# Kernel tuning notes

Measured on AMD Instinct MI355X. Metric: run time of the kernel, lower is better.

## Reference

```python
import jax, jax.numpy as jnp
import numpy as np

N_HEAD = 16
ROPE_BASE = 10000.0

def _rotate_half(x):
    # matches torch: stack((-x[...,1::2], x[...,::2]), -1).flatten(-2)
    x1 = x[..., ::2]
    x2 = x[..., 1::2]
    return jnp.stack((-x2, x1), axis=-1).reshape(x.shape)

def setup_inputs() -> dict:
    key = jax.random.key(0)
    ks = jax.random.split(key, 5)
    B, T, C = 4, 2048, 1024
    x = jax.random.normal(ks[0], (B, T, C), dtype=jnp.float32)
    Wq = jax.random.normal(ks[1], (C, C), dtype=jnp.float32) * 0.02
    Wk = jax.random.normal(ks[2], (C, C), dtype=jnp.float32) * 0.02
    Wv = jax.random.normal(ks[3], (C, C), dtype=jnp.float32) * 0.02
    Wp = jax.random.normal(ks[4], (C, C), dtype=jnp.float32) * 0.02
    return {"x": x, "Wq": Wq, "Wk": Wk, "Wv": Wv, "Wp": Wp, "start_pos": 0}

def reference(x, Wq, Wk, Wv, Wp, start_pos):
    B, T, C = x.shape
    H = N_HEAD
    D = C // H
    # torch Linear: out = x @ W^T
    q = jnp.einsum('btc,dc->btd', x, Wq).reshape(B, T, H, D).transpose(0, 2, 1, 3)
    k = jnp.einsum('btc,dc->btd', x, Wk).reshape(B, T, H, D).transpose(0, 2, 1, 3)
    v = jnp.einsum('btc,dc->btd', x, Wv).reshape(B, T, H, D).transpose(0, 2, 1, 3)
    # RoPE cache (cat[freqs, freqs] with interleaved rotate_half, as in source)
    inv_freq = 1.0 / (ROPE_BASE ** (jnp.arange(0, D, 2, dtype=jnp.float32) / D))
    t = jnp.arange(T, dtype=jnp.float32) + jnp.float32(start_pos)
    freqs = t[:, None] * inv_freq[None, :]          # [T, D/2]
    emb = jnp.concatenate([freqs, freqs], axis=-1)  # [T, D]
    cos = jnp.cos(emb)[None, None]                  # [1,1,T,D]
    sin = jnp.sin(emb)[None, None]
    q = q * cos + _rotate_half(q) * sin
    k = k * cos + _rotate_half(k) * sin
    att = jnp.einsum('bhqd,bhkd->bhqk', q, k) / jnp.sqrt(jnp.float32(D))
    mask = jnp.triu(jnp.ones((T, T), dtype=bool), k=1)
    att = jnp.where(mask, -jnp.inf, att)
    att = jax.nn.softmax(att, axis=-1)
    y = jnp.einsum('bhqk,bhkd->bhqd', att, v)
    y = y.transpose(0, 2, 1, 3).reshape(B, T, C)
    return jnp.einsum('btc,dc->btd', y, Wp)
```

## Files before the change

kernel.cpp:

```cpp
#include <hip/hip_runtime.h>
#include <hip/hip_bf16.h>
#include <stdint.h>

#define B_  4
#define T_  2048
#define C_  1024
#define H_  16
#define D_  64
#define BT  (B_*T_)
#define KDIM 1024

typedef __attribute__((ext_vector_type(8))) short bf16x8;
typedef __attribute__((ext_vector_type(4))) float f32x4;

__device__ __forceinline__ unsigned short f2bf(float f) {
  union { float f; unsigned u; } v; v.f = f;
  unsigned r = v.u + 0x7FFFu + ((v.u >> 16) & 1u);
  return (unsigned short)(r >> 16);
}

__device__ __forceinline__ float exp2_fast(float x) {
  float r;
  asm("v_exp_f32 %0, %1" : "=v"(r) : "v"(x));
  return r;
}

__device__ __forceinline__ void gld_lds16(const void* g, void* l) {
  __builtin_amdgcn_global_load_lds(
      (__attribute__((address_space(1))) unsigned int*)(uintptr_t)g,
      (__attribute__((address_space(3))) unsigned int*)(unsigned)(uintptr_t)l,
      16, 0, 0);
}

__global__ __launch_bounds__(256) void k_convert(
    const float* __restrict__ x,  const float* __restrict__ wq,
    const float* __restrict__ wk, const float* __restrict__ wv,
    const float* __restrict__ wp,
    unsigned short* __restrict__ xb, unsigned short* __restrict__ wcat,
    unsigned short* __restrict__ wpb)
{
  const int NX = BT*C_/4;
  const int NW = C_*C_/4;
  const int TOT = NX + 4*NW;
  for (int i = blockIdx.x*blockDim.x + threadIdx.x; i < TOT; i += gridDim.x*blockDim.x) {
    const float4* src; unsigned short* dst; int idx;
    if (i < NX)                { src = (const float4*)x;  dst = xb;            idx = i; }
    else {
      int j = i - NX;
      if (j < NW)              { src = (const float4*)wq; dst = wcat;          idx = j; }
      else if (j < 2*NW)       { src = (const float4*)wk; dst = wcat + C_*C_;  idx = j - NW; }
      else if (j < 3*NW)       { src = (const float4*)wv; dst = wcat + 2*C_*C_;idx = j - 2*NW; }
      else                     { src = (const float4*)wp; dst = wpb;           idx = j - 3*NW; }
    }
    float4 v = src[idx];
    ushort4 o; o.x = f2bf(v.x); o.y = f2bf(v.y); o.z = f2bf(v.z); o.w = f2bf(v.w);
    *(ushort4*)(dst + (size_t)idx*4) = o;
  }
}

__global__ __launch_bounds__(256) void k_rope_tab(
    const int* __restrict__ start_pos, float* __restrict__ cosT, float* __restrict__ sinT)
{
  int i = blockIdx.x*blockDim.x + threadIdx.x;
  if (i >= T_*D_) return;
  int t = i >> 6, j = i & 63;
  float inv = exp2f(-(float)(j & 31) * (13.287712379549449f / 32.0f));
  float ang = (float)(t + start_pos[0]) * inv;
  cosT[i] = cosf(ang);
  sinT[i] = sinf(ang);
}

__global__ __launch_bounds__(1024, 4) void k_gemm256(
    const unsigned short* __restrict__ A, const unsigned short* __restrict__ Bw,
    unsigned short* __restrict__ qb, unsigned short* __restrict__ kb,
    unsigned short* __restrict__ vt,
    const float* __restrict__ cosT, const float* __restrict__ sinT)
{
  __shared__ __attribute__((aligned(16))) char smem[114688];
  const int tid = threadIdx.x, l = tid & 63, w = tid >> 6;
  const int g = l >> 4, c = l & 15;
  const int m0 = blockIdx.x * 256, n0 = blockIdx.y * 192;
  const int wr = w >> 2, wc = w & 3;
  const char* gA = (const char*)A;
  const char* gB = (const char*)Bw;

  int dstA[2]; size_t aoff[2];
#pragma unroll
  for (int j = 0; j < 2; ++j) {
    int P = j*16384 + tid*16;
    int row = P >> 7;
    int kc = ((P & 127) ^ ((row & 7) << 4)) >> 1;
    dstA[j] = P;
    aoff[j] = ((size_t)(m0 + row) * KDIM + kc) * 2;
  }
  int dstB[2]; size_t boff[2];
#pragma unroll
  for (int j = 0; j < 2; ++j) {
    int P = (j == 0) ? tid*16 : (16384 + tid*16);
    int row = P >> 7;
    int kc = ((P & 127) ^ ((row & 7) << 4)) >> 1;
    dstB[j] = P;
    boff[j] = ((size_t)(n0 + row) * KDIM + kc) * 2;
  }
  const bool bsec = (tid < 512);

  const int aB = (wr*64 + c) * 128;
  const int bB = 32768 + (wc*48 + c) * 128;
  const int xsw = (c & 7) << 4;

  f32x4 acc[4][3];
#pragma unroll
  for (int i = 0; i < 4; ++i)
#pragma unroll
    for (int j = 0; j < 3; ++j) acc[i][j] = (f32x4){0.f,0.f,0.f,0.f};

#pragma unroll
  for (int j = 0; j < 2; ++j) gld_lds16(gA + aoff[j], smem + dstA[j]);
  gld_lds16(gB + boff[0], smem + 32768 + dstB[0]);
  if (bsec) gld_lds16(gB + boff[1], smem + 32768 + dstB[1]);

  for (int t = 0; t < 16; ++t) {
    const int par = (t & 1) ? 57344 : 0;
    const int nxt = (t & 1) ? 0 : 57344;

    __syncthreads();

    if (t + 1 < 16) {
      const size_t ko = (size_t)(t + 1) * 128;
#pragma unroll
      for (int j = 0; j < 2; ++j) gld_lds16(gA + aoff[j] + ko, smem + nxt + dstA[j]);
      gld_lds16(gB + boff[0] + ko, smem + nxt + 32768 + dstB[0]);
      if (bsec) gld_lds16(gB + boff[1] + ko, smem + nxt + 32768 + dstB[1]);
    }

#pragma unroll
    for (int kk = 0; kk < 2; ++kk) {
      const int xt = (kk*64 + g*16) ^ xsw;
      bf16x8 af[4], bk[3];
#pragma unroll
      for (int ni = 0; ni < 3; ++ni)
        bk[ni] = *(const bf16x8*)(smem + par + bB + ni*2048 + xt);
#pragma unroll
      for (int mi = 0; mi < 4; ++mi)
        af[mi] = *(const bf16x8*)(smem + par + aB + mi*2048 + xt);
      __builtin_amdgcn_s_setprio(1);
#pragma unroll
      for (int mi = 0; mi < 4; ++mi)
#pragma unroll
        for (int ni = 0; ni < 3; ++ni)
          acc[mi][ni] = __builtin_amdgcn_mfma_f32_16x16x32_bf16(af[mi], bk[ni], acc[mi][ni], 0, 0, 0);
      __builtin_amdgcn_s_setprio(0);
    }
  }

#pragma unroll
  for (int mi = 0; mi < 4; ++mi) {
#pragma unroll
    for (int ni = 0; ni < 3; ++ni) {
      const int mrow0 = m0 + wr*64 + mi*16 + g*4;
      const int ncol  = n0 + wc*48 + ni*16 + c;
      const int which = ncol >> 10;
      const int d = ncol & 1023, h = d >> 6, dd = d & 63;
      const int b = mrow0 >> 11, t0 = mrow0 & 2047;
      if (which == 2) {
        ushort4 o;
        o.x = f2bf(acc[mi][ni][0]); o.y = f2bf(acc[mi][ni][1]);
        o.z = f2bf(acc[mi][ni][2]); o.w = f2bf(acc[mi][ni][3]);
        *(ushort4*)(vt + ((size_t)((b*H_ + h)*D_ + dd))*T_ + t0) = o;
      } else {
#pragma unroll
        for (int r = 0; r < 4; ++r) {
          float val = acc[mi][ni][r];
          float partner = __shfl_xor(val, 1);
          float rot = (dd & 1) ? partner : -partner;
          float cv = cosT[(t0 + r)*64 + dd], sv = sinT[(t0 + r)*64 + dd];
          float o = val*cv + rot*sv;
          size_t oidx = (((size_t)(b*H_ + h))*T_ + (t0 + r))*D_ + dd;
          if (which == 0) qb[oidx] = f2bf(o * 0.180336879f);
          else            kb[oidx] = f2bf(o);
        }
      }
    }
  }
}

__global__ __launch_bounds__(512, 4) void k_gemm1(
    const unsigned short* __restrict__ A, const unsigned short* __restrict__ Bw,
    float* __restrict__ outF)
{
  __shared__ __attribute__((aligned(16))) char smem[65536];
  const int tid = threadIdx.x, l = tid & 63, w = tid >> 6;
  const int g = l >> 4, c = l & 15;
  const int m0 = blockIdx.x * 128, n0 = blockIdx.y * 128;
  const int wr = w >> 2, wc = w & 3;
  const char* gA = (const char*)A;
  const char* gB = (const char*)Bw;

  int dstP[2]; size_t aoff[2], boff[2];
#pragma unroll
  for (int j = 0; j < 2; ++j) {
    int P = j*8192 + tid*16;
    int row = P >> 7;
    int kc = ((P & 127) ^ ((row & 7) << 4)) >> 1;
    dstP[j] = P;
    aoff[j] = ((size_t)(m0 + row) * KDIM + kc) * 2;
    boff[j] = ((size_t)(n0 + row) * KDIM + kc) * 2;
  }

  const int aB = (wr*64 + c) * 128;
  const int bB = 16384 + (wc*32 + c) * 128;
  const int xsw = (c & 7) << 4;

  f32x4 acc[4][2];
#pragma unroll
  for (int i = 0; i < 4; ++i)
#pragma unroll
    for (int j = 0; j < 2; ++j) acc[i][j] = (f32x4){0.f,0.f,0.f,0.f};

#pragma unroll
  for (int j = 0; j < 2; ++j) {
    gld_lds16(gA + aoff[j], smem + dstP[j]);
    gld_lds16(gB + boff[j], smem + 16384 + dstP[j]);
  }

  for (int t = 0; t < 16; ++t) {
    const int par = (t & 1) << 15;
    const int nxt = par ^ 32768;

    __syncthreads();

    if (t + 1 < 16) {
      const size_t ko = (size_t)(t + 1) * 128;
#pragma unroll
      for (int j = 0; j < 2; ++j) {
        gld_lds16(gA + aoff[j] + ko, smem + nxt + dstP[j]);
        gld_lds16(gB + boff[j] + ko, smem + nxt + 16384 + dstP[j]);
      }
    }

#pragma unroll
    for (int kk = 0; kk < 2; ++kk) {
      const int xt = (kk*64 + g*16) ^ xsw;
      bf16x8 af[4], bk[2];
#pragma unroll
      for (int ni = 0; ni < 2; ++ni)
        bk[ni] = *(const bf16x8*)(smem + par + bB + ni*2048 + xt);
#pragma unroll
      for (int mi = 0; mi < 4; ++mi)
        af[mi] = *(const bf16x8*)(smem + par + aB + mi*2048 + xt);
      __builtin_amdgcn_s_setprio(1);
#pragma unroll
      for (int mi = 0; mi < 4; ++mi)
#pragma unroll
        for (int ni = 0; ni < 2; ++ni)
          acc[mi][ni] = __builtin_amdgcn_mfma_f32_16x16x32_bf16(af[mi], bk[ni], acc[mi][ni], 0, 0, 0);
      __builtin_amdgcn_s_setprio(0);
    }
  }

#pragma unroll
  for (int mi = 0; mi < 4; ++mi) {
#pragma unroll
    for (int ni = 0; ni < 2; ++ni) {
      const int mrow0 = m0 + wr*64 + mi*16 + g*4;
      const int ncol  = n0 + wc*32 + ni*16 + c;
#pragma unroll
      for (int r = 0; r < 4; ++r)
        outF[(size_t)(mrow0 + r) * 1024 + ncol] = acc[mi][ni][r];
    }
  }
}

__global__ __launch_bounds__(512) void k_attn(
    const unsigned short* __restrict__ qb, const unsigned short* __restrict__ kb,
    const unsigned short* __restrict__ vt, unsigned short* __restrict__ yb)
{
  __shared__ __attribute__((aligned(16))) char smem[49152];
  const int tid = threadIdx.x, l = tid & 63, w = tid >> 6;
  const int g = l >> 4, c = l & 15;
  const int bh = blockIdx.x;
  const int pidx = blockIdx.y;
  const size_t bhO = (size_t)bh * T_ * D_;
  const int pbase = 32768 + w*2048;
  const int b = bh >> 4, h = bh & 15;

  bf16x8 vones;
#pragma unroll
  for (int i = 0; i < 8; ++i) vones[i] = (short)0x3F80;

  const char* srcK; const char* srcV; int dstP2;
  {
    int P = w*1024 + l*16;
    int row = P >> 7;
    int Lb = P ^ ((row & 7) << 4);
    int col = (Lb & 127) >> 1;
    dstP2 = P;
    srcK = (const char*)(kb + bhO) + ((size_t)row*D_ + col)*2;
    srcV = (const char*)(vt + bhO) + ((size_t)row*T_ + col)*2;
  }

  for (int half = 0; half < 2; ++half) {
    const int qt = half ? pidx : (15 - pidx);
    const int q0 = qt * 128;
    const int q0w = q0 + w*16;

    bf16x8 aq[2];
#pragma unroll
    for (int kc = 0; kc < 2; ++kc)
      aq[kc] = *(const bf16x8*)(qb + bhO + (size_t)(q0w + c)*D_ + kc*32 + g*8);

    f32x4 po[4];
    f32x4 ls;
    float mrun = -1e30f;
#pragma unroll
    for (int nd = 0; nd < 4; ++nd) po[nd] = (f32x4){0.f,0.f,0.f,0.f};
    ls = (f32x4){0.f,0.f,0.f,0.f};

    const int nkt = (q0 + 128) >> 6;

    gld_lds16(srcK, smem + dstP2);
    gld_lds16(srcV, smem + 8192 + dstP2);
    asm volatile("s_waitcnt vmcnt(0)" ::: "memory");
    __builtin_amdgcn_s_barrier();
    __builtin_amdgcn_sched_barrier(0);

    for (int it = 0; it < nkt; ++it) {
      const int kv0 = it * 64;
      const int cur = (it & 1) * 16384;
      const bool staging = (it + 1 < nkt);

      if (staging) {
        const int wb = 16384 - cur;
        gld_lds16(srcK + (size_t)(kv0 + 64) * 128, smem + wb + dstP2);
        gld_lds16(srcV + (size_t)(kv0 + 64) * 2,   smem + wb + 8192 + dstP2);
      }

      if (kv0 < q0w + 16) {
        f32x4 st[4];
#pragma unroll
        for (int ni = 0; ni < 4; ++ni) st[ni] = (f32x4){0.f,0.f,0.f,0.f};
        __builtin_amdgcn_s_setprio(1);
#pragma unroll
        for (int kk = 0; kk < 2; ++kk) {
          bf16x8 bk[4];
#pragma unroll
          for (int ni = 0; ni < 4; ++ni) {
            int kn = ni*16 + c;
            int Lb = kn*128 + (kk*32 + g*8)*2;
            bk[ni] = *(const bf16x8*)(smem + cur + (Lb ^ ((kn & 7) << 4)));
          }
#pragma unroll
          for (int ni = 0; ni < 4; ++ni)
            st[ni] = __builtin_amdgcn_mfma_f32_16x16x32_bf16(bk[ni], aq[kk], st[ni], 0, 0, 0);
        }
        __builtin_amdgcn_s_setprio(0);

        if (kv0 + 64 > q0w) {
          const int qq = q0w + c;
#pragma unroll
          for (int ni = 0; ni < 4; ++ni)
#pragma unroll
            for (int r = 0; r < 4; ++r) {
              int kvv = kv0 + ni*16 + g*4 + r;
              if (kvv > qq) st[ni][r] = -1e30f;
            }
        }

        {
          float mn[4];
#pragma unroll
          for (int ni = 0; ni < 4; ++ni)
            mn[ni] = fmaxf(fmaxf(st[ni][0], st[ni][1]), fmaxf(st[ni][2], st[ni][3]));
          float mt = fmaxf(fmaxf(mn[0], mn[1]), fmaxf(mn[2], mn[3]));
          mt = fmaxf(mt, __shfl_xor(mt, 16));
          mt = fmaxf(mt, __shfl_xor(mt, 32));
          float m_use = mrun;
          if (__any(mt > m_use + 8.f)) {
            float mnew = fmaxf(m_use, mt);
            float alpha = exp2_fast(m_use - mnew);
            mrun = mnew;
            m_use = mnew;
#pragma unroll
            for (int r = 0; r < 4; ++r) ls[r] *= alpha;
#pragma unroll
            for (int nd = 0; nd < 4; ++nd)
#pragma unroll
              for (int r = 0; r < 4; ++r) po[nd][r] *= alpha;
          }
#pragma unroll
          for (int ni = 0; ni < 4; ++ni)
#pragma unroll
            for (int r = 0; r < 4; ++r)
              st[ni][r] = exp2_fast(st[ni][r] - m_use);
        }

        {
          const int row = c;
          const int sw = (row & 7) << 4;
          const int rb = pbase + row*128;
#pragma unroll
          for (int ni = 0; ni < 4; ++ni) {
            unsigned u0, u1;
            asm("v_cvt_pk_bf16_f32 %0, %1, %2" : "=v"(u0) : "v"(st[ni][0]), "v"(st[ni][1]));
            asm("v_cvt_pk_bf16_f32 %0, %1, %2" : "=v"(u1) : "v"(st[ni][2]), "v"(st[ni][3]));
            int Lb = (ni*16 + g*4) * 2;
            uint2 uu; uu.x = u0; uu.y = u1;
            *(uint2*)(smem + rb + (Lb ^ sw)) = uu;
          }
        }

        __builtin_amdgcn_s_setprio(1);
#pragma unroll
        for (int kk = 0; kk < 2; ++kk) {
          bf16x8 pb;
          {
            int pr = c;
            int Lb = pr*128 + (kk*32 + g*8)*2;
            pb = *(const bf16x8*)(smem + pbase + (Lb ^ ((pr & 7) << 4)));
          }
          ls = __builtin_amdgcn_mfma_f32_16x16x32_bf16(vones, pb, ls, 0, 0, 0);
          bf16x8 bv[4];
#pragma unroll
          for (int nd = 0; nd < 4; ++nd) {
            int vr = nd*16 + c;
            int Lb = vr*128 + (kk*32 + g*8)*2;
            bv[nd] = *(const bf16x8*)(smem + cur + 8192 + (Lb ^ ((vr & 7) << 4)));
          }
#pragma unroll
          for (int nd = 0; nd < 4; ++nd)
            po[nd] = __builtin_amdgcn_mfma_f32_16x16x32_bf16(bv[nd], pb, po[nd], 0, 0, 0);
        }
        __builtin_amdgcn_s_setprio(0);
      }

      if (staging) { asm volatile("s_waitcnt vmcnt(0)" ::: "memory"); }
      __builtin_amdgcn_s_barrier();
      __builtin_amdgcn_sched_barrier(0);
    }

    {
      float inv = 1.f / ls[0];
      int t = q0w + c;
#pragma unroll
      for (int nd = 0; nd < 4; ++nd) {
        ushort4 o;
        o.x = f2bf(po[nd][0] * inv);
        o.y = f2bf(po[nd][1] * inv);
        o.z = f2bf(po[nd][2] * inv);
        o.w = f2bf(po[nd][3] * inv);
        *(ushort4*)(yb + ((size_t)b*T_ + t)*C_ + h*64 + nd*16 + g*4) = o;
      }
    }
  }
}

extern "C" void kernel_launch(void* const* d_in, const int* in_sizes, int n_in,
                              void* d_out, int out_size, void* d_ws, size_t ws_size,
                              hipStream_t stream)
{
  const float* x  = (const float*)d_in[0];
  const float* Wq = (const float*)d_in[1];
  const float* Wk = (const float*)d_in[2];
  const float* Wv = (const float*)d_in[3];
  const float* Wp = (const float*)d_in[4];
  const int*   sp = (const int*)d_in[5];
  float* out = (float*)d_out;

  char* ws = (char*)d_ws;
  unsigned short* xb   = (unsigned short*)(ws);
  unsigned short* wcat = (unsigned short*)(ws + 16777216);
  unsigned short* wpb  = (unsigned short*)(ws + 23068672);
  unsigned short* qb   = (unsigned short*)(ws + 25165824);
  unsigned short* kb   = (unsigned short*)(ws + 41943040);
  unsigned short* vt   = (unsigned short*)(ws + 58720256);
  unsigned short* yb   = (unsigned short*)(ws + 75497472);
  float* cosT = (float*)(ws + 92274688);
  float* sinT = (float*)(ws + 92798976);

  k_convert<<<dim3(2048), dim3(256), 0, stream>>>(x, Wq, Wk, Wv, Wp, xb, wcat, wpb);
  k_rope_tab<<<dim3(512), dim3(256), 0, stream>>>(sp, cosT, sinT);
  k_gemm256<<<dim3(32, 16), dim3(1024), 0, stream>>>(xb, wcat, qb, kb, vt, cosT, sinT);
  k_attn<<<dim3(64, 8), dim3(512), 0, stream>>>(qb, kb, vt, yb);
  k_gemm1<<<dim3(64, 8), dim3(512), 0, stream>>>(yb, wpb, out);
}
```

Measured before the change: 161.0 us.

## Give each attention wave 32 query rows and drop paired-tile balancing

Each attention block now handles one 256-row query tile instead of two balanced 128-row tiles. Each wave owns two 16-row subtiles, so every K and V fragment read from shared memory feeds twice as many MFMAs. Per-wave shared memory for the probability buffer doubles and the block's shared allocation grows to 64KB. The cost is more accumulator registers and the loss of the front/back pairing that evened out causal work across blocks; tiles are now issued heaviest first instead.

```diff
diff --git a/kernel.cpp b/kernel.cpp
--- a/kernel.cpp
+++ b/kernel.cpp
@@ -275,13 +275,13 @@
     const unsigned short* __restrict__ qb, const unsigned short* __restrict__ kb,
     const unsigned short* __restrict__ vt, unsigned short* __restrict__ yb)
 {
-  __shared__ __attribute__((aligned(16))) char smem[49152];
+  __shared__ __attribute__((aligned(16))) char smem[65536];
   const int tid = threadIdx.x, l = tid & 63, w = tid >> 6;
   const int g = l >> 4, c = l & 15;
   const int bh = blockIdx.x;
-  const int pidx = blockIdx.y;
+  const int qt = 7 - (int)blockIdx.y;
   const size_t bhO = (size_t)bh * T_ * D_;
-  const int pbase = 32768 + w*2048;
+  const int pbase = 32768 + w*4096;
   const int b = bh >> 4, h = bh & 15;
 
   bf16x8 vones;
@@ -299,157 +299,175 @@
     srcV = (const char*)(vt + bhO) + ((size_t)row*T_ + col)*2;
   }
 
-  for (int half = 0; half < 2; ++half) {
-    const int qt = half ? pidx : (15 - pidx);
-    const int q0 = qt * 128;
-    const int q0w = q0 + w*16;
-
-    bf16x8 aq[2];
+  const int q0 = qt * 256;
+  const int q0w = q0 + w*32;
+
+  bf16x8 aq[2][2];
+#pragma unroll
+  for (int mi = 0; mi < 2; ++mi)
 #pragma unroll
     for (int kc = 0; kc < 2; ++kc)
-      aq[kc] = *(const bf16x8*)(qb + bhO + (size_t)(q0w + c)*D_ + kc*32 + g*8);
-
-    f32x4 po[4];
-    f32x4 ls;
-    float mrun = -1e30f;
-#pragma unroll
-    for (int nd = 0; nd < 4; ++nd) po[nd] = (f32x4){0.f,0.f,0.f,0.f};
-    ls = (f32x4){0.f,0.f,0.f,0.f};
-
-    const int nkt = (q0 + 128) >> 6;
-
-    gld_lds16(srcK, smem + dstP2);
-    gld_lds16(srcV, smem + 8192 + dstP2);
-    asm volatile("s_waitcnt vmcnt(0)" ::: "memory");
+      aq[mi][kc] = *(const bf16x8*)(qb + bhO + (size_t)(q0w + mi*16 + c)*D_ + kc*32 + g*8);
+
+  f32x4 po[4][2];
+  f32x4 ls[2];
+  float mrun[2];
+#pragma unroll
+  for (int nd = 0; nd < 4; ++nd)
+#pragma unroll
+    for (int mi = 0; mi < 2; ++mi) po[nd][mi] = (f32x4){0.f,0.f,0.f,0.f};
+  ls[0] = (f32x4){0.f,0.f,0.f,0.f}; ls[1] = (f32x4){0.f,0.f,0.f,0.f};
+  mrun[0] = mrun[1] = -1e30f;
+
+  const int nkt = (q0 + 256) >> 6;
+
+  gld_lds16(srcK, smem + dstP2);
+  gld_lds16(srcV, smem + 8192 + dstP2);
+  asm volatile("s_waitcnt vmcnt(0)" ::: "memory");
+  __builtin_amdgcn_s_barrier();
+  __builtin_amdgcn_sched_barrier(0);
+
+  for (int it = 0; it < nkt; ++it) {
+    const int kv0 = it * 64;
+    const int cur = (it & 1) * 16384;
+    const bool staging = (it + 1 < nkt);
+
+    if (staging) {
+      const int wb = 16384 - cur;
+      gld_lds16(srcK + (size_t)(kv0 + 64) * 128, smem + wb + dstP2);
+      gld_lds16(srcV + (size_t)(kv0 + 64) * 2,   smem + wb + 8192 + dstP2);
+    }
+
+    if (kv0 < q0w + 32) {
+      f32x4 st[4][2];
+#pragma unroll
+      for (int ni = 0; ni < 4; ++ni)
+#pragma unroll
+        for (int mi = 0; mi < 2; ++mi) st[ni][mi] = (f32x4){0.f,0.f,0.f,0.f};
+      __builtin_amdgcn_s_setprio(1);
+#pragma unroll
+      for (int kk = 0; kk < 2; ++kk) {
+        bf16x8 bk[4];
+#pragma unroll
+        for (int ni = 0; ni < 4; ++ni) {
+          int kn = ni*16 + c;
+          int Lb = kn*128 + (kk*32 + g*8)*2;
+          bk[ni] = *(const bf16x8*)(smem + cur + (Lb ^ ((kn & 7) << 4)));
+        }
+#pragma unroll
+        for (int ni = 0; ni < 4; ++ni)
+#pragma unroll
+          for (int mi = 0; mi < 2; ++mi)
+            st[ni][mi] = __builtin_amdgcn_mfma_f32_16x16x32_bf16(bk[ni], aq[mi][kk], st[ni][mi], 0, 0, 0);
+      }
+      __builtin_amdgcn_s_setprio(0);
+
+      if (kv0 + 64 > q0w) {
+#pragma unroll
+        for (int ni = 0; ni < 4; ++ni)
+#pragma unroll
+          for (int r = 0; r < 4; ++r) {
+            int kvv = kv0 + ni*16 + g*4 + r;
+#pragma unroll
+            for (int mi = 0; mi < 2; ++mi) {
+              int qq = q0w + mi*16 + c;
+              if (kvv > qq) st[ni][mi][r] = -1e30f;
+            }
+          }
+      }
+
+#pragma unroll
+      for (int mi = 0; mi < 2; ++mi) {
+        float mn[4];
+#pragma unroll
+        for (int ni = 0; ni < 4; ++ni)
+          mn[ni] = fmaxf(fmaxf(st[ni][mi][0], st[ni][mi][1]),
+                         fmaxf(st[ni][mi][2], st[ni][mi][3]));
+        float mt = fmaxf(fmaxf(mn[0], mn[1]), fmaxf(mn[2], mn[3]));
+        mt = fmaxf(mt, __shfl_xor(mt, 16));
+        mt = fmaxf(mt, __shfl_xor(mt, 32));
+        float m_use = mrun[mi];
+        if (__any(mt > m_use + 8.f)) {
+          float mnew = fmaxf(m_use, mt);
+          float alpha = exp2_fast(m_use - mnew);
+          mrun[mi] = mnew;
+          m_use = mnew;
+#pragma unroll
+          for (int r = 0; r < 4; ++r) ls[mi][r] *= alpha;
+#pragma unroll
+          for (int nd = 0; nd < 4; ++nd)
+#pragma unroll
+            for (int r = 0; r < 4; ++r) po[nd][mi][r] *= alpha;
+        }
+#pragma unroll
+        for (int ni = 0; ni < 4; ++ni)
+#pragma unroll
+          for (int r = 0; r < 4; ++r)
+            st[ni][mi][r] = exp2_fast(st[ni][mi][r] - m_use);
+      }
+
+#pragma unroll
+      for (int mi = 0; mi < 2; ++mi) {
+        const int row = mi*16 + c;
+        const int sw = (row & 7) << 4;
+        const int rb = pbase + row*128;
+#pragma unroll
+        for (int ni = 0; ni < 4; ++ni) {
+          unsigned u0, u1;
+          asm("v_cvt_pk_bf16_f32 %0, %1, %2" : "=v"(u0) : "v"(st[ni][mi][0]), "v"(st[ni][mi][1]));
+          asm("v_cvt_pk_bf16_f32 %0, %1, %2" : "=v"(u1) : "v"(st[ni][mi][2]), "v"(st[ni][mi][3]));
+          int Lb = (ni*16 + g*4) * 2;
+          uint2 uu; uu.x = u0; uu.y = u1;
+          *(uint2*)(smem + rb + (Lb ^ sw)) = uu;
+        }
+      }
+
+      __builtin_amdgcn_s_setprio(1);
+#pragma unroll
+      for (int kk = 0; kk < 2; ++kk) {
+        bf16x8 pb[2];
+#pragma unroll
+        for (int mi = 0; mi < 2; ++mi) {
+          int pr = mi*16 + c;
+          int Lb = pr*128 + (kk*32 + g*8)*2;
+          pb[mi] = *(const bf16x8*)(smem + pbase + (Lb ^ ((pr & 7) << 4)));
+        }
+#pragma unroll
+        for (int mi = 0; mi < 2; ++mi)
+          ls[mi] = __builtin_amdgcn_mfma_f32_16x16x32_bf16(vones, pb[mi], ls[mi], 0, 0, 0);
+        bf16x8 bv[4];
+#pragma unroll
+        for (int nd = 0; nd < 4; ++nd) {
+          int vr = nd*16 + c;
+          int Lb = vr*128 + (kk*32 + g*8)*2;
+          bv[nd] = *(const bf16x8*)(smem + cur + 8192 + (Lb ^ ((vr & 7) << 4)));
+        }
+#pragma unroll
+        for (int nd = 0; nd < 4; ++nd)
+#pragma unroll
+          for (int mi = 0; mi < 2; ++mi)
+            po[nd][mi] = __builtin_amdgcn_mfma_f32_16x16x32_bf16(bv[nd], pb[mi], po[nd][mi], 0, 0, 0);
+      }
+      __builtin_amdgcn_s_setprio(0);
+    }
+
+    if (staging) { asm volatile("s_waitcnt vmcnt(0)" ::: "memory"); }
     __builtin_amdgcn_s_barrier();
     __builtin_amdgcn_sched_barrier(0);
-
-    for (int it = 0; it < nkt; ++it) {
-      const int kv0 = it * 64;
-      const int cur = (it & 1) * 16384;
-      const bool staging = (it + 1 < nkt);
-
-      if (staging) {
-        const int wb = 16384 - cur;
-        gld_lds16(srcK + (size_t)(kv0 + 64) * 128, smem + wb + dstP2);
-        gld_lds16(srcV + (size_t)(kv0 + 64) * 2,   smem + wb + 8192 + dstP2);
-      }
-
-      if (kv0 < q0w + 16) {
-        f32x4 st[4];
-#pragma unroll
-        for (int ni = 0; ni < 4; ++ni) st[ni] = (f32x4){0.f,0.f,0.f,0.f};
-        __builtin_amdgcn_s_setprio(1);
-#pragma unroll
-        for (int kk = 0; kk < 2; ++kk) {
-          bf16x8 bk[4];
-#pragma unroll
-          for (int ni = 0; ni < 4; ++ni) {
-            int kn = ni*16 + c;
-            int Lb = kn*128 + (kk*32 + g*8)*2;
-            bk[ni] = *(const bf16x8*)(smem + cur + (Lb ^ ((kn & 7) << 4)));
-          }
-#pragma unroll
-          for (int ni = 0; ni < 4; ++ni)
-            st[ni] = __builtin_amdgcn_mfma_f32_16x16x32_bf16(bk[ni], aq[kk], st[ni], 0, 0, 0);
-        }
-        __builtin_amdgcn_s_setprio(0);
-
-        if (kv0 + 64 > q0w) {
-          const int qq = q0w + c;
-#pragma unroll
-          for (int ni = 0; ni < 4; ++ni)
-#pragma unroll
-            for (int r = 0; r < 4; ++r) {
-              int kvv = kv0 + ni*16 + g*4 + r;
-              if (kvv > qq) st[ni][r] = -1e30f;
-            }
-        }
-
-        {
-          float mn[4];
-#pragma unroll
-          for (int ni = 0; ni < 4; ++ni)
-            mn[ni] = fmaxf(fmaxf(st[ni][0], st[ni][1]), fmaxf(st[ni][2], st[ni][3]));
-          float mt = fmaxf(fmaxf(mn[0], mn[1]), fmaxf(mn[2], mn[3]));
-          mt = fmaxf(mt, __shfl_xor(mt, 16));
-          mt = fmaxf(mt, __shfl_xor(mt, 32));
-          float m_use = mrun;
-          if (__any(mt > m_use + 8.f)) {
-            float mnew = fmaxf(m_use, mt);
-            float alpha = exp2_fast(m_use - mnew);
-            mrun = mnew;
-            m_use = mnew;
-#pragma unroll
-            for (int r = 0; r < 4; ++r) ls[r] *= alpha;
-#pragma unroll
-            for (int nd = 0; nd < 4; ++nd)
-#pragma unroll
-              for (int r = 0; r < 4; ++r) po[nd][r] *= alpha;
-          }
-#pragma unroll
-          for (int ni = 0; ni < 4; ++ni)
-#pragma unroll
-            for (int r = 0; r < 4; ++r)
-              st[ni][r] = exp2_fast(st[ni][r] - m_use);
-        }
-
-        {
-          const int row = c;
-          const int sw = (row & 7) << 4;
-          const int rb = pbase + row*128;
-#pragma unroll
-          for (int ni = 0; ni < 4; ++ni) {
-            unsigned u0, u1;
-            asm("v_cvt_pk_bf16_f32 %0, %1, %2" : "=v"(u0) : "v"(st[ni][0]), "v"(st[ni][1]));
-            asm("v_cvt_pk_bf16_f32 %0, %1, %2" : "=v"(u1) : "v"(st[ni][2]), "v"(st[ni][3]));
-            int Lb = (ni*16 + g*4) * 2;
-            uint2 uu; uu.x = u0; uu.y = u1;
-            *(uint2*)(smem + rb + (Lb ^ sw)) = uu;
-          }
-        }
-
-        __builtin_amdgcn_s_setprio(1);
-#pragma unroll
-        for (int kk = 0; kk < 2; ++kk) {
-          bf16x8 pb;
-          {
-            int pr = c;
-            int Lb = pr*128 + (kk*32 + g*8)*2;
-            pb = *(const bf16x8*)(smem + pbase + (Lb ^ ((pr & 7) << 4)));
-          }
-          ls = __builtin_amdgcn_mfma_f32_16x16x32_bf16(vones, pb, ls, 0, 0, 0);
-          bf16x8 bv[4];
-#pragma unroll
-          for (int nd = 0; nd < 4; ++nd) {
-            int vr = nd*16 + c;
-            int Lb = vr*128 + (kk*32 + g*8)*2;
-            bv[nd] = *(const bf16x8*)(smem + cur + 8192 + (Lb ^ ((vr & 7) << 4)));
-          }
-#pragma unroll
-          for (int nd = 0; nd < 4; ++nd)
-            po[nd] = __builtin_amdgcn_mfma_f32_16x16x32_bf16(bv[nd], pb, po[nd], 0, 0, 0);
-        }
-        __builtin_amdgcn_s_setprio(0);
-      }
-
-      if (staging) { asm volatile("s_waitcnt vmcnt(0)" ::: "memory"); }
-      __builtin_amdgcn_s_barrier();
-      __builtin_amdgcn_sched_barrier(0);
-    }
-
-    {
-      float inv = 1.f / ls[0];
-      int t = q0w + c;
-#pragma unroll
-      for (int nd = 0; nd < 4; ++nd) {
-        ushort4 o;
-        o.x = f2bf(po[nd][0] * inv);
-        o.y = f2bf(po[nd][1] * inv);
-        o.z = f2bf(po[nd][2] * inv);
-        o.w = f2bf(po[nd][3] * inv);
-        *(ushort4*)(yb + ((size_t)b*T_ + t)*C_ + h*64 + nd*16 + g*4) = o;
-      }
+  }
+
+#pragma unroll
+  for (int mi = 0; mi < 2; ++mi) {
+    float inv = 1.f / ls[mi][0];
+    int t = q0w + mi*16 + c;
+#pragma unroll
+    for (int nd = 0; nd < 4; ++nd) {
+      ushort4 o;
+      o.x = f2bf(po[nd][mi][0] * inv);
+      o.y = f2bf(po[nd][mi][1] * inv);
+      o.z = f2bf(po[nd][mi][2] * inv);
+      o.w = f2bf(po[nd][mi][3] * inv);
+      *(ushort4*)(yb + ((size_t)b*T_ + t)*C_ + h*64 + nd*16 + g*4) = o;
     }
   }
 }
```

New measurement: 166.0 us. 1.03x slower.
